# Kernel optimization log

Measured on AMD Instinct MI355X. Metric: run time of the kernel, lower is better.

## Reference

```python
import jax, jax.numpy as jnp
import numpy as np

B, DIM, H, W = 32, 512, 48, 24


def conv1x1(x, w, b):
    # x: [B,C,H,W], w: [O,C], b: [O]  (torch Conv2d 1x1 weight squeezed)
    return jnp.einsum('bchw,oc->bohw', x, w) + b[None, :, None, None]


def setup_inputs() -> dict:
    key = jax.random.key(0)
    ks = jax.random.split(key, 14)
    s = 0.02
    inp = {
        'x': jax.random.normal(ks[0], (B, DIM, H, W), jnp.float32),
        'x_h': jax.random.normal(ks[1], (B, DIM, H, W), jnp.float32),
        'Wg': jax.random.normal(ks[2], (DIM, DIM), jnp.float32) * s,
        'bg': jax.random.normal(ks[3], (DIM,), jnp.float32) * s,
        'Wt': jax.random.normal(ks[4], (DIM, DIM), jnp.float32) * s,
        'bt': jax.random.normal(ks[5], (DIM,), jnp.float32) * s,
        'Wp': jax.random.normal(ks[6], (DIM, DIM), jnp.float32) * s,
        'bp': jax.random.normal(ks[7], (DIM,), jnp.float32) * s,
        'Ww': jax.random.normal(ks[8], (DIM, DIM), jnp.float32) * s,
        'bw': jax.random.normal(ks[9], (DIM,), jnp.float32) * s,
        'gamma': jax.random.normal(ks[10], (DIM,), jnp.float32) * 0.1,
        'beta': jax.random.normal(ks[11], (DIM,), jnp.float32) * 0.1,
        'run_mean': jax.random.normal(ks[12], (DIM,), jnp.float32) * 0.1,
        'run_var': jax.random.uniform(ks[13], (DIM,), jnp.float32, 0.5, 1.5),
    }
    return inp


def reference(x, x_h, Wg, bg, Wt, bt, Wp, bp, Ww, bw, gamma, beta, run_mean, run_var):
    Bsz, dim = x.shape[0], Wg.shape[0]
    g_x = conv1x1(x_h, Wg, bg).reshape(Bsz, dim, -1)      # [B,dim,N]
    theta_x = conv1x1(x, Wt, bt).reshape(Bsz, dim, -1)    # [B,dim,N]
    phi_x = conv1x1(x_h, Wp, bp).reshape(Bsz, dim, -1)    # [B,dim,N]
    # energy[b,i,j] = sum_n theta[b,i,n] * phi[b,j,n]  -> channel attention [B,dim,dim]
    energy = jnp.einsum('bin,bjn->bij', theta_x, phi_x)
    attention = energy / dim  # energy.size(-1) == dim
    y = jnp.einsum('bij,bjn->bin', attention, g_x).reshape(Bsz, dim, *x_h.shape[2:])
    W_y = conv1x1(y, Ww, bw)
    # BatchNorm2d in eval mode
    inv = gamma / jnp.sqrt(run_var + 1e-5)
    W_y = (W_y - run_mean[None, :, None, None]) * inv[None, :, None, None] + beta[None, :, None, None]
    return W_y + x
```

## Files before the change

kernel.cpp:

```cpp
#include <hip/hip_runtime.h>
#include <stdint.h>

typedef short short8 __attribute__((ext_vector_type(8)));
typedef float f32x4 __attribute__((ext_vector_type(4)));
typedef unsigned short u16;
typedef unsigned int u32;

struct alignas(8) U16x4 { u16 x, y, z, w; };

__device__ __forceinline__ u16 f2bf(float f) {
  u32 u = __float_as_uint(f);
  u += 0x7fffu + ((u >> 16) & 1u);
  return (u16)(u >> 16);
}
__device__ __forceinline__ float bf2f(u16 v) {
  return __uint_as_float(((u32)v) << 16);
}

__device__ __forceinline__ void gld_lds16(const u16* g, u16* l) {
  __builtin_amdgcn_global_load_lds((const __attribute__((address_space(1))) u32*)g,
                                   (__attribute__((address_space(3))) u32*)l,
                                   16, 0, 0);
}

__device__ __forceinline__ void mfma16x16x32(f32x4& c, short8 a, short8 b) {
  asm("v_mfma_f32_16x16x32_bf16 %0, %1, %2, %0" : "+v"(c) : "v"(a), "v"(b));
}

__device__ __forceinline__ float wave_red(float v) {
  for (int off = 32; off; off >>= 1) v += __shfl_down(v, off);
  return v;
}

template<int EPI>
__global__ void __launch_bounds__(256, 2) gemm_abt(
                         const u16* __restrict__ A, int64_t Abs,
                         const u16* __restrict__ Bt, int64_t Bbs,
                         void* __restrict__ Cptr, int64_t Cbs,
                         int M, int N, int K,
                         const float* __restrict__ v1,
                         const float* __restrict__ v2,
                         const float* __restrict__ v3,
                         const float* __restrict__ v4,
                         const float* __restrict__ xres) {
  constexpr int BM = 128, BN = 128, BK = 64;
  __shared__ u16 As[2][BM * BK];
  __shared__ u16 Bs[2][BN * BK];

  int bx, by, b;
  if (gridDim.z == 1) {
    const int nbx = N >> 7;
    const int bpb = nbx * (M >> 7);
    const int id = blockIdx.x;
    const int xcd = id & 7, rest = id >> 3;
    b = xcd + 8 * (rest / bpb);
    const int wi = rest % bpb;
    by = wi / nbx; bx = wi % nbx;
  } else {
    bx = blockIdx.x; by = blockIdx.y; b = blockIdx.z;
  }

  const u16* Ab = A + (int64_t)b * Abs;
  const u16* Bb = Bt + (int64_t)b * Bbs;
  const int brow = by * BM, bcol = bx * BN;
  const int tid = threadIdx.x, lane = tid & 63, w = tid >> 6;
  const int wr = w >> 1, wc = w & 1;

  f32x4 acc[4][4] = {};

  const int sr = tid >> 3;
  const int scs = ((tid & 7) ^ (sr & 7)) * 8;
  u16* lA0 = &As[0][sr * BK + (tid & 7) * 8];
  u16* lB0 = &Bs[0][sr * BK + (tid & 7) * 8];
  const u16* gA = Ab + (int64_t)(brow + sr) * K + scs;
  const u16* gB = Bb + (int64_t)(bcol + sr) * K + scs;

  const int la16 = lane & 15;
  const int kg = (lane >> 4) * 8;
  const int swz = (la16 & 7) * 8;
  const int nt = K / BK;

#pragma unroll
  for (int i = 0; i < 4; ++i) {
    gld_lds16(gA + (int64_t)i * 32 * K, lA0 + i * 32 * BK);
    gld_lds16(gB + (int64_t)i * 32 * K, lB0 + i * 32 * BK);
  }

  for (int t = 0; t < nt; ++t) {
    __builtin_amdgcn_s_barrier();
    if (t + 1 < nt) {
      const int nb = (t + 1) & 1;
      const int k0 = (t + 1) * BK;
      u16* la = lA0 + nb * BM * BK;
      u16* lb = lB0 + nb * BN * BK;
#pragma unroll
      for (int i = 0; i < 4; ++i) {
        gld_lds16(gA + (int64_t)i * 32 * K + k0, la + i * 32 * BK);
        gld_lds16(gB + (int64_t)i * 32 * K + k0, lb + i * 32 * BK);
      }
      asm volatile("s_waitcnt vmcnt(8)" ::: "memory");
    } else {
      asm volatile("s_waitcnt vmcnt(0)" ::: "memory");
    }
    __builtin_amdgcn_s_barrier();
    __builtin_amdgcn_sched_barrier(0);
    const u16* as = As[t & 1];
    const u16* bs = Bs[t & 1];
#pragma unroll
    for (int kk = 0; kk < 2; ++kk) {
      short8 af[4], bf[4];
      const int kc = (kk * 32 + kg) ^ swz;
#pragma unroll
      for (int m = 0; m < 4; ++m)
        af[m] = *(const short8*)&as[(wr * 64 + m * 16 + la16) * BK + kc];
#pragma unroll
      for (int n = 0; n < 4; ++n)
        bf[n] = *(const short8*)&bs[(wc * 64 + n * 16 + la16) * BK + kc];
#pragma unroll
      for (int m = 0; m < 4; ++m)
#pragma unroll
        for (int n = 0; n < 4; ++n)
          mfma16x16x32(acc[m][n], af[m], bf[n]);
    }
  }
  asm volatile("s_nop 7\n\ts_nop 7");

  const int r0 = brow + wr * 64 + (lane >> 4) * 4;
  const int c0 = bcol + wc * 64 + la16;
  const int64_t b512 = (int64_t)b * 512;

  if (EPI == 4) {
    float* Cb = (float*)Cptr + (int64_t)b * Cbs;
    const float* xb = xres + (int64_t)b * Cbs;
#pragma unroll
    for (int m = 0; m < 4; ++m) {
#pragma unroll
      for (int r = 0; r < 4; ++r) {
        const int row = r0 + m * 16 + r;
        const float scl = v1[row], shf = v2[b512 + row];
#pragma unroll
        for (int n = 0; n < 4; ++n) {
          const int col = c0 + n * 16;
          Cb[(int64_t)row * N + col] = acc[m][n][r] * scl + shf + xb[(int64_t)row * N + col];
        }
      }
    }
  } else {
    u16* Cb = (u16*)Cptr + (int64_t)b * Cbs;
#pragma unroll
    for (int m = 0; m < 4; ++m) {
#pragma unroll
      for (int r = 0; r < 4; ++r) {
        const int row = r0 + m * 16 + r;
        float a1 = 0.f, a3 = 0.f;
        if (EPI == 6) { a1 = v1[b512 + row]; a3 = v3[row]; }
#pragma unroll
        for (int n = 0; n < 4; ++n) {
          const int col = c0 + n * 16;
          float v = acc[m][n][r];
          if (EPI == 6) v += a1 * v2[col] + a3 * v4[b512 + col];
          Cb[(int64_t)row * N + col] = f2bf(v);
        }
      }
    }
  }
}

__global__ void cvt_row(const float* __restrict__ in, u16* __restrict__ out,
                        float* __restrict__ rowsum) {
  const int64_t row = blockIdx.x;
  const float4* ib = (const float4*)(in + row * 1152);
  U16x4* ob = (U16x4*)(out + row * 1152);
  float s = 0.f;
  for (int i = threadIdx.x; i < 288; i += 256) {
    float4 v = ib[i];
    s += v.x + v.y + v.z + v.w;
    U16x4 o = {f2bf(v.x), f2bf(v.y), f2bf(v.z), f2bf(v.w)};
    ob[i] = o;
  }
  s = wave_red(s);
  __shared__ float red[4];
  if ((threadIdx.x & 63) == 0) red[threadIdx.x >> 6] = s;
  __syncthreads();
  if (threadIdx.x == 0) rowsum[row] = red[0] + red[1] + red[2] + red[3];
}

__global__ void prep_xh(const float* __restrict__ xh, u16* __restrict__ xhB,
                        u16* __restrict__ xhT, float* __restrict__ rxh_part) {
  __shared__ float tl[32][33];
  const int b = blockIdx.z;
  const int n0 = blockIdx.x * 32, c0 = blockIdx.y * 32;
  const float* ib = xh + (int64_t)b * 589824;
  const int tr = threadIdx.x >> 3, tc = (threadIdx.x & 7) * 4;
  const float4 v = *(const float4*)&ib[(int64_t)(c0 + tr) * 1152 + n0 + tc];
  tl[tr][tc] = v.x; tl[tr][tc + 1] = v.y; tl[tr][tc + 2] = v.z; tl[tr][tc + 3] = v.w;
  U16x4 o = {f2bf(v.x), f2bf(v.y), f2bf(v.z), f2bf(v.w)};
  *(U16x4*)&xhB[(int64_t)b * 589824 + (int64_t)(c0 + tr) * 1152 + n0 + tc] = o;
  __syncthreads();
  U16x4 ot = {f2bf(tl[tc][tr]), f2bf(tl[tc + 1][tr]),
              f2bf(tl[tc + 2][tr]), f2bf(tl[tc + 3][tr])};
  *(U16x4*)&xhT[(int64_t)b * 589824 + (int64_t)(n0 + tr) * 512 + c0 + tc] = ot;
  if (threadIdx.x < 32) {
    float s = 0;
#pragma unroll
    for (int c = 0; c < 32; ++c) s += tl[threadIdx.x][c];
    rxh_part[(n0 >> 5) * 16384 + b * 512 + c0 + threadIdx.x] = s;
  }
}

__global__ void transpose_cvt4(const float* __restrict__ s0, const float* __restrict__ s1,
                               const float* __restrict__ s2, const float* __restrict__ s3,
                               u16* __restrict__ d0, u16* __restrict__ d1,
                               u16* __restrict__ d2, u16* __restrict__ d3) {
  const int z = blockIdx.z;
  const float* in = z == 0 ? s0 : z == 1 ? s1 : z == 2 ? s2 : s3;
  u16* out = z == 0 ? d0 : z == 1 ? d1 : z == 2 ? d2 : d3;
  __shared__ float t[32][33];
  const int n0 = blockIdx.x * 32, c0 = blockIdx.y * 32;
  const int tr = threadIdx.x >> 3, tc = (threadIdx.x & 7) * 4;
  const float4 v = *(const float4*)&in[(int64_t)(c0 + tr) * 512 + n0 + tc];
  t[tr][tc] = v.x; t[tr][tc + 1] = v.y; t[tr][tc + 2] = v.z; t[tr][tc + 3] = v.w;
  __syncthreads();
  U16x4 o;
  o.x = f2bf(t[tc][tr]); o.y = f2bf(t[tc + 1][tr]);
  o.z = f2bf(t[tc + 2][tr]); o.w = f2bf(t[tc + 3][tr]);
  *(U16x4*)&out[(int64_t)(n0 + tr) * 512 + c0 + tc] = o;
}

__global__ void cvt_kernel(const float* __restrict__ in, u16* __restrict__ out, int n4) {
  const int i = blockIdx.x * 256 + threadIdx.x;
  if (i < n4) {
    const float4 v = ((const float4*)in)[i];
    U16x4 o = {f2bf(v.x), f2bf(v.y), f2bf(v.z), f2bf(v.w)};
    ((U16x4*)out)[i] = o;
  }
}

__global__ void k_misc(const float* __restrict__ rxh_part, float* __restrict__ rxh,
                       const float* __restrict__ gamma, const float* __restrict__ beta,
                       const float* __restrict__ mean, const float* __restrict__ var,
                       const float* __restrict__ bw,
                       const float* __restrict__ bp, const float* __restrict__ bg,
                       float* __restrict__ sc2, float* __restrict__ shift0,
                       float* __restrict__ s2) {
  if (blockIdx.x < 64) {
    const int i = blockIdx.x * 256 + threadIdx.x;
    float s = 0;
#pragma unroll 4
    for (int p = 0; p < 36; ++p) s += rxh_part[p * 16384 + i];
    rxh[i] = s;
  } else {
    for (int c = threadIdx.x; c < 512; c += 256) {
      const float sc = gamma[c] * rsqrtf(var[c] + 1e-5f);
      sc2[c] = sc * (1.0f / 512.0f);
      shift0[c] = (bw[c] - mean[c]) * sc + beta[c];
    }
    if (threadIdx.x < 64) {
      float p = 0;
      for (int k = threadIdx.x; k < 512; k += 64) p += bp[k] * bg[k];
      p = wave_red(p);
      if (threadIdx.x == 0) s2[0] = p;
    }
  }
}

__global__ void k_mv1(const float* __restrict__ Wp, const float* __restrict__ Wt,
                      const float* __restrict__ Ww,
                      const u16* __restrict__ WpT, const u16* __restrict__ WgT,
                      const float* __restrict__ bg, const float* __restrict__ bt,
                      const float* __restrict__ bp,
                      const float* __restrict__ rx, const float* __restrict__ rxh,
                      float* __restrict__ sigphi, float* __restrict__ tau2,
                      float* __restrict__ h1, float* __restrict__ w1,
                      float* __restrict__ c2) {
  const int wid = blockIdx.x * 4 + (threadIdx.x >> 6);
  const int lane = threadIdx.x & 63;
  float dot = 0;
  if (wid < 16384) {
    const int b = wid >> 9, t = wid & 511;
    const float* wr = Wp + (int64_t)t * 512;
    const float* vr = rxh + b * 512;
#pragma unroll
    for (int k = 0; k < 8; ++k) dot += wr[lane + k * 64] * vr[lane + k * 64];
    dot = wave_red(dot);
    if (lane == 0) sigphi[wid] = dot;
  } else if (wid < 32768) {
    const int r = wid - 16384, b = r >> 9, t = r & 511;
    const float* wr = Wt + (int64_t)t * 512;
    const float* vr = rx + b * 512;
#pragma unroll
    for (int k = 0; k < 8; ++k) dot += wr[lane + k * 64] * vr[lane + k * 64];
    dot = wave_red(dot);
    if (lane == 0) tau2[r] = dot + 1152.0f * bt[t];
  } else if (wid < 33280) {
    const int j = wid - 32768;
    const u16* wr = WpT + (int64_t)j * 512;
#pragma unroll
    for (int k = 0; k < 8; ++k) dot += bf2f(wr[lane + k * 64]) * bg[lane + k * 64];
    dot = wave_red(dot);
    if (lane == 0) h1[j] = dot;
  } else if (wid < 33792) {
    const int c = wid - 33280;
    const float* wr = Ww + (int64_t)c * 512;
#pragma unroll
    for (int k = 0; k < 8; ++k) dot += wr[lane + k * 64] * bt[lane + k * 64];
    dot = wave_red(dot);
    if (lane == 0) w1[c] = dot;
  } else {
    const int e = wid - 33792;
    const u16* wr = WgT + (int64_t)e * 512;
#pragma unroll
    for (int k = 0; k < 8; ++k) dot += bf2f(wr[lane + k * 64]) * bp[lane + k * 64];
    dot = wave_red(dot);
    if (lane == 0) c2[e] = dot;
  }
}

__global__ void k_mv2(const u16* __restrict__ WgT, const float* __restrict__ Ww,
                      const float* __restrict__ bg,
                      const float* __restrict__ sigphi, const float* __restrict__ tau2,
                      float* __restrict__ c1, float* __restrict__ w2,
                      float* __restrict__ s1) {
  const int wid = blockIdx.x * 4 + (threadIdx.x >> 6);
  const int lane = threadIdx.x & 63;
  float dot = 0;
  if (wid < 16384) {
    const int b = wid >> 9, t = wid & 511;
    const u16* wr = WgT + (int64_t)t * 512;
    const float* vr = sigphi + b * 512;
#pragma unroll
    for (int k = 0; k < 8; ++k) dot += bf2f(wr[lane + k * 64]) * vr[lane + k * 64];
    dot = wave_red(dot);
    if (lane == 0) c1[wid] = dot;
  } else if (wid < 32768) {
    const int r = wid - 16384, b = r >> 9, t = r & 511;
    const float* wr = Ww + (int64_t)t * 512;
    const float* vr = tau2 + b * 512;
#pragma unroll
    for (int k = 0; k < 8; ++k) dot += wr[lane + k * 64] * vr[lane + k * 64];
    dot = wave_red(dot);
    if (lane == 0) w2[r] = dot;
  } else if (wid < 32800) {
    const int b = wid - 32768;
    const float* vr = sigphi + b * 512;
#pragma unroll
    for (int k = 0; k < 8; ++k) dot += vr[lane + k * 64] * bg[lane + k * 64];
    dot = wave_red(dot);
    if (lane == 0) s1[b] = dot;
  }
}

__global__ void k_shiftv(const u16* __restrict__ R, const float* __restrict__ h1,
                         const float* __restrict__ w1, const float* __restrict__ w2,
                         const float* __restrict__ s1, const float* __restrict__ s2,
                         const float* __restrict__ sc2, const float* __restrict__ shift0,
                         float* __restrict__ shiftv) {
  const int wid = blockIdx.x * 4 + (threadIdx.x >> 6);
  const int lane = threadIdx.x & 63;
  const int b = wid >> 9, c = wid & 511;
  const u16* rr = R + (int64_t)b * 262144 + (int64_t)c * 512;
  float dot = 0;
#pragma unroll
  for (int k = 0; k < 8; ++k) dot += bf2f(rr[lane + k * 64]) * h1[lane + k * 64];
  dot = wave_red(dot);
  if (lane == 0)
    shiftv[wid] = sc2[c] * (dot + s1[b] * w1[c] + s2[0] * w2[wid]) + shift0[c];
}

extern "C" void kernel_launch(void* const* d_in, const int* in_sizes, int n_in,
                              void* d_out, int out_size, void* d_ws, size_t ws_size,
                              hipStream_t stream) {
  const float* x     = (const float*)d_in[0];
  const float* x_h   = (const float*)d_in[1];
  const float* Wg    = (const float*)d_in[2];
  const float* bg    = (const float*)d_in[3];
  const float* Wt    = (const float*)d_in[4];
  const float* bt    = (const float*)d_in[5];
  const float* Wp    = (const float*)d_in[6];
  const float* bp    = (const float*)d_in[7];
  const float* Ww    = (const float*)d_in[8];
  const float* bw    = (const float*)d_in[9];
  const float* gamma = (const float*)d_in[10];
  const float* beta  = (const float*)d_in[11];
  const float* rmean = (const float*)d_in[12];
  const float* rvar  = (const float*)d_in[13];
  float* out = (float*)d_out;

  const int Bsz = 32, D = 512, N = 1152;
  const int64_t DN = (int64_t)D * N;
  const int64_t DD = (int64_t)D * D;

  char* ws = (char*)d_ws;
  const size_t KB = 1024, MB = 1048576;
  u16* WtT  = (u16*)(ws + 0);
  u16* WpT  = (u16*)(ws + 512 * KB);
  u16* WwB  = (u16*)(ws + 1 * MB);
  u16* WgT  = (u16*)(ws + 1 * MB + 512 * KB);
  u16* WaB  = (u16*)(ws + 2 * MB);
  u16* WbTB = (u16*)(ws + 2 * MB + 512 * KB);
  u16* WwT  = (u16*)(ws + 3 * MB);
  float* rx     = (float*)(ws + 3 * MB + 512 * KB);
  float* rxh    = (float*)(ws + 3 * MB + 576 * KB);
  float* sigphi = (float*)(ws + 3 * MB + 640 * KB);
  float* tau2   = (float*)(ws + 3 * MB + 704 * KB);
  float* c1     = (float*)(ws + 3 * MB + 768 * KB);
  float* w2     = (float*)(ws + 3 * MB + 832 * KB);
  float* shiftv = (float*)(ws + 3 * MB + 896 * KB);
  float* h1     = (float*)(ws + 3 * MB + 960 * KB);
  float* w1     = (float*)(ws + 3 * MB + 962 * KB);
  float* c2     = (float*)(ws + 3 * MB + 964 * KB);
  float* sc2    = (float*)(ws + 3 * MB + 968 * KB);
  float* shift0 = (float*)(ws + 3 * MB + 970 * KB);
  float* s1     = (float*)(ws + 3 * MB + 972 * KB);
  float* s2     = (float*)(ws + 3 * MB + 974 * KB);
  u16* xB  = (u16*)(ws + 4 * MB);
  u16* xhB = (u16*)(ws + 40 * MB);
  u16* xhT = (u16*)(ws + 76 * MB);
  u16* SD1 = (u16*)(ws + 112 * MB);
  u16* SD2 = (u16*)(ws + 130 * MB);
  float* rxh_part = (float*)(ws + 148 * MB);

  cvt_row<<<dim3(Bsz * D), 256, 0, stream>>>(x, xB, rx);
  prep_xh<<<dim3(36, 16, Bsz), 256, 0, stream>>>(x_h, xhB, xhT, rxh_part);
  transpose_cvt4<<<dim3(16, 16, 4), 256, 0, stream>>>(Wt, Wp, Wg, Ww, WtT, WpT, WgT, WwT);
  cvt_kernel<<<dim3(D * D / 4 / 256), 256, 0, stream>>>(Ww, WwB, D * D / 4);
  k_misc<<<dim3(65), 256, 0, stream>>>(rxh_part, rxh, gamma, beta, rmean, rvar, bw,
                                       bp, bg, sc2, shift0, s2);
  k_mv1<<<dim3(8576), 256, 0, stream>>>(Wp, Wt, Ww, WpT, WgT, bg, bt, bp, rx, rxh,
                                        sigphi, tau2, h1, w1, c2);
  k_mv2<<<dim3(8200), 256, 0, stream>>>(WgT, Ww, bg, sigphi, tau2, c1, w2, s1);
  gemm_abt<0><<<dim3(4, 4, 2), 256, 0, stream>>>(
      WwB, DD, WtT, DD, WaB, DD, D, D, D, nullptr, nullptr, nullptr, nullptr, nullptr);

  gemm_abt<0><<<dim3(16 * Bsz), 256, 0, stream>>>(
      xhB, DN, xB, DN, SD1, DD, D, D, N, nullptr, nullptr, nullptr, nullptr, nullptr);
  gemm_abt<0><<<dim3(16 * Bsz), 256, 0, stream>>>(
      WaB, 0, SD1, DD, SD2, DD, D, D, D, nullptr, nullptr, nullptr, nullptr, nullptr);
  k_shiftv<<<dim3(4096), 256, 0, stream>>>(SD2, h1, w1, w2, s1, s2, sc2, shift0, shiftv);
  gemm_abt<6><<<dim3(16 * Bsz), 256, 0, stream>>>(
      SD2, DD, WbTB, 0, SD1, DD, D, D, D, w2, c2, w1, c1, nullptr);
  gemm_abt<4><<<dim3(36 * Bsz), 256, 0, stream>>>(
      SD1, DD, xhT, DN, out, DN, D, N, D, sc2, shiftv, nullptr, nullptr, x);
}
```

Baseline: 212.8 us.

## Enlarge GEMM block tile to 256x128 with 512 threads and bf16 residual

The batched GEMM kernel now uses a 256x128 block tile with 8 waves (512 threads) and a K-step of 32 instead of 64, with the LDS swizzle and load mapping adjusted to match. Each block tile is larger, so each B tile loaded is reused across more rows. The final epilogue reads the residual from the bf16 copy of x instead of fp32 x, cutting residual read traffic in half. In exchange there is twice the barrier count per K, fewer and larger blocks, and a slight loss of precision in the residual add.

```diff
diff --git a/kernel.cpp b/kernel.cpp
--- a/kernel.cpp
+++ b/kernel.cpp
@@ -33,7 +33,7 @@
 }
 
 template<int EPI>
-__global__ void __launch_bounds__(256, 2) gemm_abt(
+__global__ void __launch_bounds__(512, 2) gemm_abt(
                          const u16* __restrict__ A, int64_t Abs,
                          const u16* __restrict__ Bt, int64_t Bbs,
                          void* __restrict__ Cptr, int64_t Cbs,
@@ -42,15 +42,15 @@
                          const float* __restrict__ v2,
                          const float* __restrict__ v3,
                          const float* __restrict__ v4,
-                         const float* __restrict__ xres) {
-  constexpr int BM = 128, BN = 128, BK = 64;
+                         const u16* __restrict__ xres) {
+  constexpr int BM = 256, BN = 128, BK = 32;
   __shared__ u16 As[2][BM * BK];
   __shared__ u16 Bs[2][BN * BK];
 
   int bx, by, b;
   if (gridDim.z == 1) {
     const int nbx = N >> 7;
-    const int bpb = nbx * (M >> 7);
+    const int bpb = nbx * (M >> 8);
     const int id = blockIdx.x;
     const int xcd = id & 7, rest = id >> 3;
     b = xcd + 8 * (rest / bpb);
@@ -68,23 +68,21 @@
 
   f32x4 acc[4][4] = {};
 
-  const int sr = tid >> 3;
-  const int scs = ((tid & 7) ^ (sr & 7)) * 8;
-  u16* lA0 = &As[0][sr * BK + (tid & 7) * 8];
-  u16* lB0 = &Bs[0][sr * BK + (tid & 7) * 8];
+  const int sr = tid >> 2;
+  const int scs = ((tid & 3) ^ (sr & 3)) * 8;
+  u16* lA0 = &As[0][sr * BK + (tid & 3) * 8];
+  u16* lB0 = &Bs[0][sr * BK + (tid & 3) * 8];
   const u16* gA = Ab + (int64_t)(brow + sr) * K + scs;
   const u16* gB = Bb + (int64_t)(bcol + sr) * K + scs;
 
   const int la16 = lane & 15;
   const int kg = (lane >> 4) * 8;
-  const int swz = (la16 & 7) * 8;
+  const int kc = kg ^ ((la16 & 3) * 8);
   const int nt = K / BK;
 
-#pragma unroll
-  for (int i = 0; i < 4; ++i) {
-    gld_lds16(gA + (int64_t)i * 32 * K, lA0 + i * 32 * BK);
-    gld_lds16(gB + (int64_t)i * 32 * K, lB0 + i * 32 * BK);
-  }
+  gld_lds16(gA, lA0);
+  gld_lds16(gA + (int64_t)128 * K, lA0 + 128 * BK);
+  gld_lds16(gB, lB0);
 
   for (int t = 0; t < nt; ++t) {
     __builtin_amdgcn_s_barrier();
@@ -93,12 +91,10 @@
       const int k0 = (t + 1) * BK;
       u16* la = lA0 + nb * BM * BK;
       u16* lb = lB0 + nb * BN * BK;
-#pragma unroll
-      for (int i = 0; i < 4; ++i) {
-        gld_lds16(gA + (int64_t)i * 32 * K + k0, la + i * 32 * BK);
-        gld_lds16(gB + (int64_t)i * 32 * K + k0, lb + i * 32 * BK);
-      }
-      asm volatile("s_waitcnt vmcnt(8)" ::: "memory");
+      gld_lds16(gA + k0, la);
+      gld_lds16(gA + (int64_t)128 * K + k0, la + 128 * BK);
+      gld_lds16(gB + k0, lb);
+      asm volatile("s_waitcnt vmcnt(3)" ::: "memory");
     } else {
       asm volatile("s_waitcnt vmcnt(0)" ::: "memory");
     }
@@ -106,22 +102,18 @@
     __builtin_amdgcn_sched_barrier(0);
     const u16* as = As[t & 1];
     const u16* bs = Bs[t & 1];
-#pragma unroll
-    for (int kk = 0; kk < 2; ++kk) {
-      short8 af[4], bf[4];
-      const int kc = (kk * 32 + kg) ^ swz;
-#pragma unroll
-      for (int m = 0; m < 4; ++m)
-        af[m] = *(const short8*)&as[(wr * 64 + m * 16 + la16) * BK + kc];
+    short8 af[4], bf[4];
+#pragma unroll
+    for (int m = 0; m < 4; ++m)
+      af[m] = *(const short8*)&as[(wr * 64 + m * 16 + la16) * BK + kc];
+#pragma unroll
+    for (int n = 0; n < 4; ++n)
+      bf[n] = *(const short8*)&bs[(wc * 64 + n * 16 + la16) * BK + kc];
+#pragma unroll
+    for (int m = 0; m < 4; ++m)
 #pragma unroll
       for (int n = 0; n < 4; ++n)
-        bf[n] = *(const short8*)&bs[(wc * 64 + n * 16 + la16) * BK + kc];
-#pragma unroll
-      for (int m = 0; m < 4; ++m)
-#pragma unroll
-        for (int n = 0; n < 4; ++n)
-          mfma16x16x32(acc[m][n], af[m], bf[n]);
-    }
+        mfma16x16x32(acc[m][n], af[m], bf[n]);
   }
   asm volatile("s_nop 7\n\ts_nop 7");
 
@@ -131,7 +123,7 @@
 
   if (EPI == 4) {
     float* Cb = (float*)Cptr + (int64_t)b * Cbs;
-    const float* xb = xres + (int64_t)b * Cbs;
+    const u16* xb = xres + (int64_t)b * Cbs;
 #pragma unroll
     for (int m = 0; m < 4; ++m) {
 #pragma unroll
@@ -141,7 +133,8 @@
 #pragma unroll
         for (int n = 0; n < 4; ++n) {
           const int col = c0 + n * 16;
-          Cb[(int64_t)row * N + col] = acc[m][n][r] * scl + shf + xb[(int64_t)row * N + col];
+          Cb[(int64_t)row * N + col] =
+              acc[m][n][r] * scl + shf + bf2f(xb[(int64_t)row * N + col]);
         }
       }
     }
@@ -429,16 +422,16 @@
   k_mv1<<<dim3(8576), 256, 0, stream>>>(Wp, Wt, Ww, WpT, WgT, bg, bt, bp, rx, rxh,
                                         sigphi, tau2, h1, w1, c2);
   k_mv2<<<dim3(8200), 256, 0, stream>>>(WgT, Ww, bg, sigphi, tau2, c1, w2, s1);
-  gemm_abt<0><<<dim3(4, 4, 2), 256, 0, stream>>>(
+  gemm_abt<0><<<dim3(4, 2, 2), 512, 0, stream>>>(
       WwB, DD, WtT, DD, WaB, DD, D, D, D, nullptr, nullptr, nullptr, nullptr, nullptr);
 
-  gemm_abt<0><<<dim3(16 * Bsz), 256, 0, stream>>>(
+  gemm_abt<0><<<dim3(8 * Bsz), 512, 0, stream>>>(
       xhB, DN, xB, DN, SD1, DD, D, D, N, nullptr, nullptr, nullptr, nullptr, nullptr);
-  gemm_abt<0><<<dim3(16 * Bsz), 256, 0, stream>>>(
+  gemm_abt<0><<<dim3(8 * Bsz), 512, 0, stream>>>(
       WaB, 0, SD1, DD, SD2, DD, D, D, D, nullptr, nullptr, nullptr, nullptr, nullptr);
   k_shiftv<<<dim3(4096), 256, 0, stream>>>(SD2, h1, w1, w2, s1, s2, sc2, shift0, shiftv);
-  gemm_abt<6><<<dim3(16 * Bsz), 256, 0, stream>>>(
+  gemm_abt<6><<<dim3(8 * Bsz), 512, 0, stream>>>(
       SD2, DD, WbTB, 0, SD1, DD, D, D, D, w2, c2, w1, c1, nullptr);
-  gemm_abt<4><<<dim3(36 * Bsz), 256, 0, stream>>>(
-      SD1, DD, xhT, DN, out, DN, D, N, D, sc2, shiftv, nullptr, nullptr, x);
-}
+  gemm_abt<4><<<dim3(18 * Bsz), 512, 0, stream>>>(
+      SD1, DD, xhT, DN, out, DN, D, N, D, sc2, shiftv, nullptr, nullptr, xB);
+}
```

Result: slower. 225.2 us (+5.8%).
